# Performance work log

Measured on AMD Instinct MI355X. Metric: run time of the kernel, lower is better.

Reference implementation:

```python
import jax, jax.numpy as jnp
import numpy as np

N_NODES = 100000
N_EDGES = 1600000
D_IN = 128
D_OUT = 128
N_GRAPHS = 256


def setup_inputs() -> dict:
    key = jax.random.key(0)
    k1, k2, k3, k4 = jax.random.split(key, 4)
    H = jax.random.normal(k1, (N_NODES, D_IN), dtype=jnp.float32)
    edge_index = jax.random.randint(k2, (2, N_EDGES), 0, N_NODES, dtype=jnp.int64)
    batch = jnp.sort(jax.random.randint(k3, (N_NODES,), 0, N_GRAPHS, dtype=jnp.int64))
    # Kaiming-normal init: std = sqrt(2 / fan_in)
    W = jax.random.normal(k4, (D_IN, D_OUT), dtype=jnp.float32) * np.float32(np.sqrt(2.0 / D_IN))
    return {"H": H, "edge_index": edge_index, "batch": batch, "W": W}


def reference(H, edge_index, batch, W):
    N = H.shape[0]
    src, dst = edge_index[0], edge_index[1]
    # message passing: gather source features, scatter_add into destinations
    agg = jax.ops.segment_sum(H[src], dst, num_segments=N)  # [N, D]
    out = H + agg
    # virtual node: per-graph mean, broadcast back to nodes
    sums = jax.ops.segment_sum(out, batch, num_segments=N_GRAPHS)            # [G, D]
    counts = jax.ops.segment_sum(jnp.ones((N, 1), out.dtype), batch,
                                 num_segments=N_GRAPHS)                       # [G, 1]
    vmean = sums / jnp.maximum(counts, 1.0)
    out = out + vmean[batch]
    # dense transform + activation
    return jax.nn.relu(out @ W)
```

## Files before the change

### kernel.cpp

```cpp
#include <hip/hip_runtime.h>

#define DIM 128
#define NGRAPH 256

#define CHUNK 512
#define CHB 9
#define MAXNB 256
#define EPB 4096
#define EPT (EPB / 256)
#define FCAP 14336

typedef __attribute__((ext_vector_type(8))) short short8;
typedef __attribute__((ext_vector_type(4))) float f32x4;

__device__ inline unsigned int bpack2(float lo, float hi) {
  unsigned int ul = __float_as_uint(lo);
  unsigned int uh = __float_as_uint(hi);
  ul = (ul + 0x7fffu + ((ul >> 16) & 1u)) >> 16;
  uh = (uh + 0x7fffu + ((uh >> 16) & 1u)) & 0xffff0000u;
  return ul | uh;
}

__global__ __launch_bounds__(256) void k_h2b(const float4* __restrict__ in,
    uint2* __restrict__ ob, int n4) {
  int i = blockIdx.x * 256 + threadIdx.x;
  if (i < n4) {
    float4 a = in[i];
    uint2 r;
    r.x = bpack2(a.x, a.y);
    r.y = bpack2(a.z, a.w);
    ob[i] = r;
  }
}

__global__ __launch_bounds__(256) void k_bhist(const int* __restrict__ dst,
    unsigned short* __restrict__ bh, int E) {
  __shared__ unsigned int hist[MAXNB];
  int blk = blockIdx.x, t = threadIdx.x;
  hist[t] = 0;
  __syncthreads();
  int base = blk * EPB;
#pragma unroll
  for (int i = 0; i < EPT; ++i) {
    int e = base + i * 256 + t;
    if (e < E) atomicAdd(&hist[((unsigned)dst[e]) >> CHB], 1);
  }
  __syncthreads();
  bh[(size_t)blk * MAXNB + t] = (unsigned short)hist[t];
}

__global__ __launch_bounds__(256) void k_bscan(unsigned short* __restrict__ bh,
    unsigned int* __restrict__ btot, int NBLK) {
  __shared__ unsigned int tmp[256];
  int b = blockIdx.x, t = threadIdx.x;
  int i0 = 2 * t, i1 = 2 * t + 1;
  unsigned int a0 = (i0 < NBLK) ? bh[(size_t)i0 * MAXNB + b] : 0u;
  unsigned int a1 = (i1 < NBLK) ? bh[(size_t)i1 * MAXNB + b] : 0u;
  unsigned int ps = a0 + a1;
  tmp[t] = ps;
  __syncthreads();
  for (int off = 1; off < 256; off <<= 1) {
    unsigned int x = (t >= off) ? tmp[t - off] : 0u;
    __syncthreads();
    tmp[t] += x;
    __syncthreads();
  }
  unsigned int ex = tmp[t] - ps;
  if (i0 < NBLK) bh[(size_t)i0 * MAXNB + b] = (unsigned short)ex;
  if (i1 < NBLK) bh[(size_t)i1 * MAXNB + b] = (unsigned short)(ex + a0);
  if (t == 255) btot[b] = tmp[255];
}

__global__ __launch_bounds__(256) void k_bscan2(const unsigned int* __restrict__ btot,
    unsigned int* __restrict__ bbase, int* __restrict__ offs, int N, int E) {
  __shared__ unsigned int s[256];
  int t = threadIdx.x;
  unsigned int v = btot[t];
  s[t] = v;
  __syncthreads();
  for (int off = 1; off < 256; off <<= 1) {
    unsigned int x = (t >= off) ? s[t - off] : 0u;
    __syncthreads();
    s[t] += x;
    __syncthreads();
  }
  bbase[t] = s[t] - v;
  if (t == 255) { bbase[256] = s[255]; offs[N] = E; }
}

__global__ __launch_bounds__(256) void k_part(const int* __restrict__ src,
    const int* __restrict__ dst, const unsigned short* __restrict__ bh,
    const unsigned int* __restrict__ bbase, unsigned int* __restrict__ pack, int E) {
  __shared__ unsigned int hist[MAXNB];
  __shared__ unsigned int sc[MAXNB];
  __shared__ unsigned int gbase[MAXNB];
  __shared__ unsigned int lpack[EPB];
  __shared__ unsigned short lbkt[EPB];
  __shared__ unsigned int totS;
  int blk = blockIdx.x, t = threadIdx.x;
  hist[t] = 0;
  __syncthreads();

  int base = blk * EPB;
  unsigned int pk[EPT];
  int bk[EPT];
  unsigned int rk[EPT];
#pragma unroll
  for (int i = 0; i < EPT; ++i) {
    int e = base + i * 256 + t;
    if (e < E) {
      unsigned int s = (unsigned)src[e], d = (unsigned)dst[e];
      pk[i] = (s << CHB) | (d & (CHUNK - 1));
      int b = (int)(d >> CHB);
      bk[i] = b;
      rk[i] = atomicAdd(&hist[b], 1u);
    } else {
      bk[i] = -1;
    }
  }
  __syncthreads();

  unsigned int c = hist[t];
  sc[t] = c;
  __syncthreads();
  for (int off = 1; off < 256; off <<= 1) {
    unsigned int x = (t >= off) ? sc[t - off] : 0u;
    __syncthreads();
    sc[t] += x;
    __syncthreads();
  }
  if (t == 255) totS = sc[255];
  hist[t] = sc[t] - c;
  gbase[t] = bbase[t] + (unsigned int)bh[(size_t)blk * MAXNB + t];
  __syncthreads();

#pragma unroll
  for (int i = 0; i < EPT; ++i) {
    if (bk[i] >= 0) {
      unsigned int slot = hist[bk[i]] + rk[i];
      lpack[slot] = pk[i];
      lbkt[slot] = (unsigned short)bk[i];
    }
  }
  __syncthreads();

  unsigned int tot = totS;
  for (unsigned int s = t; s < tot; s += 256) {
    int b = lbkt[s];
    unsigned int local = s - hist[b];
    pack[gbase[b] + local] = lpack[s];
  }
}

__global__ __launch_bounds__(256) void k_fine(unsigned int* __restrict__ pack,
    const unsigned int* __restrict__ bbase, int* __restrict__ offs, int N) {
  __shared__ unsigned int lp[FCAP];
  __shared__ unsigned int cnt[CHUNK];
  __shared__ unsigned int cur[CHUNK];
  __shared__ unsigned int tmp[256];
  int b = blockIdx.x, t = threadIdx.x;
  unsigned int lo = bbase[b], hi = bbase[b + 1];
  int n = (int)(hi - lo);
  if (n > FCAP) n = FCAP;
  cnt[2 * t] = 0; cnt[2 * t + 1] = 0;
  __syncthreads();
  for (int i = t; i < n; i += 256) {
    unsigned int p = pack[lo + i];
    lp[i] = p;
    atomicAdd(&cnt[p & (CHUNK - 1)], 1u);
  }
  __syncthreads();
  unsigned int c0 = cnt[2 * t], c1 = cnt[2 * t + 1];
  unsigned int ps = c0 + c1;
  tmp[t] = ps;
  __syncthreads();
  for (int off = 1; off < 256; off <<= 1) {
    unsigned int x = (t >= off) ? tmp[t - off] : 0u;
    __syncthreads();
    tmp[t] += x;
    __syncthreads();
  }
  unsigned int ex = tmp[t] - ps;
  cur[2 * t] = ex;
  cur[2 * t + 1] = ex + c0;
  __syncthreads();
  int nb0 = b * CHUNK;
#pragma unroll
  for (int j = t; j < CHUNK; j += 256) {
    int node = nb0 + j;
    if (node < N) offs[node] = (int)(lo + cur[j]);
  }
  __syncthreads();
  for (int i = t; i < n; i += 256) {
    unsigned int p = lp[i];
    unsigned int r = atomicAdd(&cur[p & (CHUNK - 1)], 1u);
    pack[lo + r] = p;
  }
}

__device__ inline void bacc(uint2 v, float4& a) {
  a.x += __uint_as_float(v.x << 16);
  a.y += __uint_as_float(v.x & 0xffff0000u);
  a.z += __uint_as_float(v.y << 16);
  a.w += __uint_as_float(v.y & 0xffff0000u);
}

__global__ __launch_bounds__(256) void k_gatherb(const float* __restrict__ H,
    const uint2* __restrict__ Hb, const int* __restrict__ offs,
    const unsigned int* __restrict__ pack, float* __restrict__ out, int n) {
  int gid = blockIdx.x * 256 + threadIdx.x;
  int node = gid >> 6;
  if (node >= n) return;
  int lane = threadIdx.x & 63;
  int half = lane >> 5, q = lane & 31;
  float4 A = {0,0,0,0}, B = {0,0,0,0}, C = {0,0,0,0}, D = {0,0,0,0};
  int beg = offs[node], end = offs[node + 1];
  int j = beg + half;
  for (; j + 6 < end; j += 8) {
    uint2 v0 = Hb[(size_t)(pack[j + 0] >> CHB) * 32 + q];
    uint2 v1 = Hb[(size_t)(pack[j + 2] >> CHB) * 32 + q];
    uint2 v2 = Hb[(size_t)(pack[j + 4] >> CHB) * 32 + q];
    uint2 v3 = Hb[(size_t)(pack[j + 6] >> CHB) * 32 + q];
    bacc(v0, A); bacc(v1, B); bacc(v2, C); bacc(v3, D);
  }
  for (; j < end; j += 2) bacc(Hb[(size_t)(pack[j] >> CHB) * 32 + q], A);
  A.x += B.x + (C.x + D.x);
  A.y += B.y + (C.y + D.y);
  A.z += B.z + (C.z + D.z);
  A.w += B.w + (C.w + D.w);
  A.x += __shfl_xor(A.x, 32);
  A.y += __shfl_xor(A.y, 32);
  A.z += __shfl_xor(A.z, 32);
  A.w += __shfl_xor(A.w, 32);
  if (half == 0) {
    float4 b4 = ((const float4*)H)[(size_t)node * 32 + q];
    float4 r;
    r.x = b4.x + A.x; r.y = b4.y + A.y; r.z = b4.z + A.z; r.w = b4.w + A.w;
    ((float4*)out)[(size_t)node * 32 + q] = r;
  }
}

__global__ __launch_bounds__(256) void k_gather(const float* __restrict__ H,
    const int* __restrict__ offs, const unsigned int* __restrict__ pack,
    float* __restrict__ out, int n) {
  int gid = blockIdx.x * 256 + threadIdx.x;
  int node = gid >> 6;
  if (node >= n) return;
  int lane = threadIdx.x & 63;
  const float2* H2 = (const float2*)H;
  float2 base = H2[(size_t)node * 64 + lane];
  float2 s0 = {0.f, 0.f}, s1 = {0.f, 0.f}, s2 = {0.f, 0.f}, s3 = {0.f, 0.f};
  int beg = offs[node], end = offs[node + 1];
  int j = beg;
  for (; j + 4 <= end; j += 4) {
    int n0 = (int)(pack[j + 0] >> CHB);
    int n1 = (int)(pack[j + 1] >> CHB);
    int n2 = (int)(pack[j + 2] >> CHB);
    int n3 = (int)(pack[j + 3] >> CHB);
    float2 v0 = H2[(size_t)n0 * 64 + lane];
    float2 v1 = H2[(size_t)n1 * 64 + lane];
    float2 v2 = H2[(size_t)n2 * 64 + lane];
    float2 v3 = H2[(size_t)n3 * 64 + lane];
    s0.x += v0.x; s0.y += v0.y;
    s1.x += v1.x; s1.y += v1.y;
    s2.x += v2.x; s2.y += v2.y;
    s3.x += v3.x; s3.y += v3.y;
  }
  for (; j < end; ++j) {
    float2 v = H2[(size_t)(pack[j] >> CHB) * 64 + lane];
    s0.x += v.x; s0.y += v.y;
  }
  float2 r;
  r.x = base.x + ((s0.x + s1.x) + (s2.x + s3.x));
  r.y = base.y + ((s0.y + s1.y) + (s2.y + s3.y));
  ((float2*)out)[(size_t)node * 64 + lane] = r;
}

__global__ __launch_bounds__(256) void k_init(const float4* __restrict__ s,
                                              float4* __restrict__ d, int n4) {
  int i = blockIdx.x * 256 + threadIdx.x;
  if (i < n4) d[i] = s[i];
}

__global__ __launch_bounds__(256) void k_scatter(const float* __restrict__ H,
    const int* __restrict__ src, const int* __restrict__ dst,
    float* __restrict__ out, int nE) {
  long long idx = (long long)blockIdx.x * 256 + threadIdx.x;
  int e = (int)(idx >> 5);
  if (e >= nE) return;
  int q = (int)(idx & 31);
  int s = src[e];
  int t = dst[e];
  const float4 h = *(const float4*)(H + (size_t)s * DIM + q * 4);
  float* o = out + (size_t)t * DIM + q * 4;
  unsafeAtomicAdd(o + 0, h.x);
  unsafeAtomicAdd(o + 1, h.y);
  unsafeAtomicAdd(o + 2, h.z);
  unsafeAtomicAdd(o + 3, h.w);
}

__global__ __launch_bounds__(256) void k_vmean4(const float* __restrict__ x,
    const int* __restrict__ batch, float* __restrict__ vmean, int n) {
  int g = blockIdx.x >> 2, c = blockIdx.x & 3;
  int lo = 0, hi = n;
  while (lo < hi) { int m = (lo + hi) >> 1; if (batch[m] < g) lo = m + 1; else hi = m; }
  int start = lo;
  hi = n;
  while (lo < hi) { int m = (lo + hi) >> 1; if (batch[m] < g + 1) lo = m + 1; else hi = m; }
  int end = lo;

  int t = threadIdx.x, rg = t >> 3, s = t & 7;
  int d4 = c * 8 + s;
  const float4* x4 = (const float4*)x;
  float4 acc = {0,0,0,0};
  for (int r = start + rg; r < end; r += 32) {
    float4 v = x4[(size_t)r * 32 + d4];
    acc.x += v.x; acc.y += v.y; acc.z += v.z; acc.w += v.w;
  }
  __shared__ float4 sd[256];
  sd[t] = acc;
  __syncthreads();
  for (int off = 16; off >= 1; off >>= 1) {
    if (rg < off) {
      float4 o = sd[t + off * 8];
      acc.x += o.x; acc.y += o.y; acc.z += o.z; acc.w += o.w;
      sd[t] = acc;
    }
    __syncthreads();
  }
  if (rg == 0) {
    float cnt = fmaxf((float)(end - start), 1.0f);
    float4 r;
    r.x = acc.x / cnt; r.y = acc.y / cnt; r.z = acc.z / cnt; r.w = acc.w / cnt;
    ((float4*)vmean)[g * 32 + d4] = r;
  }
}

__global__ __launch_bounds__(256) void k_wprep(const float* __restrict__ W,
                                               uint4* __restrict__ wt) {
  int gid = blockIdx.x * 256 + threadIdx.x;
  int col = gid >> 4, chunk = gid & 15;
  float f[8];
#pragma unroll
  for (int j = 0; j < 8; ++j) f[j] = W[(chunk * 8 + j) * DIM + col];
  uint4 u;
  u.x = bpack2(f[0], f[1]);
  u.y = bpack2(f[2], f[3]);
  u.z = bpack2(f[4], f[5]);
  u.w = bpack2(f[6], f[7]);
  wt[col * 16 + (chunk ^ (col & 7))] = u;
}

__global__ __launch_bounds__(256) void k_mfma(float* __restrict__ io,
    const int* __restrict__ batch, const float* __restrict__ vmean,
    const uint4* __restrict__ wt, int n) {
  __shared__ uint4 WtL[2048];
  int tid = threadIdx.x;
#pragma unroll
  for (int j = 0; j < 8; ++j) WtL[tid + 256 * j] = wt[tid + 256 * j];
  __syncthreads();

  int wid = tid >> 6;
  int lane = tid & 63;
  int q = lane & 15, hi = lane >> 4;
  int row0 = blockIdx.x * 128 + wid * 32;

  f32x4 acc[2][8];
#pragma unroll
  for (int m = 0; m < 2; ++m)
#pragma unroll
    for (int nn = 0; nn < 8; ++nn) acc[m][nn] = (f32x4){0.f, 0.f, 0.f, 0.f};

  bool okm[2];
  const float4* xrow[2];
  const float4* vrow[2];
#pragma unroll
  for (int m = 0; m < 2; ++m) {
    int row = row0 + m * 16 + q;
    bool ok = row < n;
    okm[m] = ok;
    int g = ok ? batch[row] : 0;
    xrow[m] = (const float4*)io + (size_t)row * 32;
    vrow[m] = (const float4*)vmean + (size_t)g * 32;
  }

  for (int kk = 0; kk < 4; ++kk) {
    short8 Bf[8];
#pragma unroll
    for (int nn = 0; nn < 8; ++nn) {
      int colrow = nn * 16 + q;
      int idx = colrow * 16 + ((kk * 4 + hi) ^ (colrow & 7));
      Bf[nn] = *(short8*)&WtL[idx];
    }
    short8 Af[2];
#pragma unroll
    for (int m = 0; m < 2; ++m) {
      float4 x0 = {0,0,0,0}, x1 = {0,0,0,0};
      if (okm[m]) {
        int c = kk * 8 + hi * 2;
        float4 a0 = xrow[m][c], a1 = xrow[m][c + 1];
        float4 v0 = vrow[m][c], v1 = vrow[m][c + 1];
        x0.x = a0.x + v0.x; x0.y = a0.y + v0.y; x0.z = a0.z + v0.z; x0.w = a0.w + v0.w;
        x1.x = a1.x + v1.x; x1.y = a1.y + v1.y; x1.z = a1.z + v1.z; x1.w = a1.w + v1.w;
      }
      uint4 u;
      u.x = bpack2(x0.x, x0.y);
      u.y = bpack2(x0.z, x0.w);
      u.z = bpack2(x1.x, x1.y);
      u.w = bpack2(x1.z, x1.w);
      Af[m] = *(short8*)&u;
    }
#pragma unroll
    for (int nn = 0; nn < 8; ++nn) {
      acc[0][nn] = __builtin_amdgcn_mfma_f32_16x16x32_bf16(Af[0], Bf[nn], acc[0][nn], 0, 0, 0);
      acc[1][nn] = __builtin_amdgcn_mfma_f32_16x16x32_bf16(Af[1], Bf[nn], acc[1][nn], 0, 0, 0);
    }
  }

#pragma unroll
  for (int m = 0; m < 2; ++m) {
    int grow0 = row0 + m * 16 + hi * 4;
#pragma unroll
    for (int nn = 0; nn < 8; ++nn) {
      int gcol = nn * 16 + q;
      f32x4 c = acc[m][nn];
#pragma unroll
      for (int r = 0; r < 4; ++r) {
        int grow = grow0 + r;
        if (grow < n) io[(size_t)grow * DIM + gcol] = fmaxf(c[r], 0.f);
      }
    }
  }
}

#define TRR 64
__global__ __launch_bounds__(256) void k_gemm(float* __restrict__ io,
    const int* __restrict__ batch, const float* __restrict__ vmean,
    const float* __restrict__ W, int n) {
  __shared__ float xs[TRR][DIM + 1];
  __shared__ float Wl[DIM][64];
  int tid = threadIdx.x;
  int row0 = blockIdx.x * TRR;

  for (int i = tid; i < TRR * 32; i += 256) {
    int r = i >> 5, c4 = i & 31;
    int row = row0 + r;
    float4 a;
    if (row < n) {
      int g = batch[row];
      float4 xv = *((const float4*)(io + (size_t)row * DIM) + c4);
      float4 vv = *((const float4*)(vmean + (size_t)g * DIM) + c4);
      a.x = xv.x + vv.x; a.y = xv.y + vv.y; a.z = xv.z + vv.z; a.w = xv.w + vv.w;
    } else {
      a.x = a.y = a.z = a.w = 0.f;
    }
    xs[r][c4 * 4 + 0] = a.x;
    xs[r][c4 * 4 + 1] = a.y;
    xs[r][c4 * 4 + 2] = a.z;
    xs[r][c4 * 4 + 3] = a.w;
  }

  int cg = tid & 15;
  int rg = tid >> 4;
  float acc[4][4];

  for (int jh = 0; jh < 2; ++jh) {
    __syncthreads();
    for (int i = tid; i < DIM * 16; i += 256) {
      int k = i >> 4, c4 = i & 15;
      *(float4*)&Wl[k][c4 * 4] =
          *(const float4*)(W + (size_t)k * DIM + jh * 64 + c4 * 4);
    }
    __syncthreads();

#pragma unroll
    for (int a = 0; a < 4; ++a)
#pragma unroll
      for (int b = 0; b < 4; ++b) acc[a][b] = 0.f;

    for (int k = 0; k < DIM; ++k) {
      float4 wv = *(const float4*)&Wl[k][cg * 4];
#pragma unroll
      for (int a = 0; a < 4; ++a) {
        float xv = xs[rg * 4 + a][k];
        acc[a][0] += xv * wv.x;
        acc[a][1] += xv * wv.y;
        acc[a][2] += xv * wv.z;
        acc[a][3] += xv * wv.w;
      }
    }

#pragma unroll
    for (int a = 0; a < 4; ++a) {
      int row = row0 + rg * 4 + a;
      if (row < n) {
        float4 o;
        o.x = fmaxf(acc[a][0], 0.f);
        o.y = fmaxf(acc[a][1], 0.f);
        o.z = fmaxf(acc[a][2], 0.f);
        o.w = fmaxf(acc[a][3], 0.f);
        *(float4*)(io + (size_t)row * DIM + jh * 64 + cg * 4) = o;
      }
    }
  }
}

extern "C" void kernel_launch(void* const* d_in, const int* in_sizes, int n_in,
                              void* d_out, int out_size, void* d_ws, size_t ws_size,
                              hipStream_t stream) {
  const float* H     = (const float*)d_in[0];
  const int*   ei    = (const int*)d_in[1];
  const int*   batch = (const int*)d_in[2];
  const float* W     = (const float*)d_in[3];
  float* out = (float*)d_out;

  int N = in_sizes[0] / DIM;
  int E = in_sizes[1] / 2;
  const int* src = ei;
  const int* dst = ei + E;

  int NB   = (N + CHUNK - 1) >> CHB;
  int NBLK = (E + EPB - 1) / EPB;

  size_t o = 0;
  auto carve = [&](size_t bytes) -> void* {
    void* p = (char*)d_ws + o;
    o = (o + bytes + 255) & ~(size_t)255;
    return p;
  };
  unsigned int*   pack  = (unsigned int*)carve((size_t)E * 4);
  int*            offs  = (int*)carve(((size_t)N + 1) * 4);
  unsigned short* bh    = (unsigned short*)carve((size_t)NBLK * MAXNB * 2);
  unsigned int*   btot  = (unsigned int*)carve(MAXNB * 4);
  unsigned int*   bbase = (unsigned int*)carve((MAXNB + 1) * 4);
  size_t o_csr = o;
  uint2*          Hb    = (uint2*)carve((size_t)N * DIM * 2);
  size_t o_bf = o;
  uint4*          wt    = (uint4*)carve((size_t)DIM * DIM * 2);
  size_t o_wt = o;
  float* vmean = (float*)bh;

  bool csr_ok = (o_csr <= ws_size) && (NB >= 1) && (NB <= MAXNB) &&
                (NBLK <= 512) && ((size_t)NBLK * MAXNB * 2 >= (size_t)NGRAPH * DIM * 4) &&
                (E / NB <= 8192);
  bool bf_ok = csr_ok && (o_bf <= ws_size);
  bool wt_ok = bf_ok && (o_wt <= ws_size) && (DIM == 128);

  if (csr_ok) {
    k_bhist<<<NBLK, 256, 0, stream>>>(dst, bh, E);
    k_bscan<<<MAXNB, 256, 0, stream>>>(bh, btot, NBLK);
    k_bscan2<<<1, 256, 0, stream>>>(btot, bbase, offs, N, E);
    k_part<<<NBLK, 256, 0, stream>>>(src, dst, bh, bbase, pack, E);
    k_fine<<<NB, 256, 0, stream>>>(pack, bbase, offs, N);
    long long gthreads = (long long)N * 64;
    if (bf_ok) {
      int n4 = N * DIM / 4;
      k_h2b<<<(n4 + 255) / 256, 256, 0, stream>>>((const float4*)H, Hb, n4);
      k_gatherb<<<(int)((gthreads + 255) / 256), 256, 0, stream>>>(H, Hb, offs, pack, out, N);
    } else {
      k_gather<<<(int)((gthreads + 255) / 256), 256, 0, stream>>>(H, offs, pack, out, N);
    }
  } else {
    vmean = (float*)d_ws;
    int n4 = N * DIM / 4;
    k_init<<<(n4 + 255) / 256, 256, 0, stream>>>((const float4*)H, (float4*)out, n4);
    long long sthreads = (long long)E * 32;
    k_scatter<<<(int)((sthreads + 255) / 256), 256, 0, stream>>>(H, src, dst, out, E);
  }

  k_vmean4<<<NGRAPH * 4, 256, 0, stream>>>(out, batch, vmean, N);

  if (wt_ok) {
    k_wprep<<<8, 256, 0, stream>>>(W, wt);
    k_mfma<<<(N + 127) / 128, 256, 0, stream>>>(out, batch, vmean, wt, N);
  } else {
    k_gemm<<<(N + TRR - 1) / TRR, 256, 0, stream>>>(out, batch, vmean, W, N);
  }
}
```

Baseline: 168.2 us.

## Split bf16 feature gather into two column-half passes and fuse histogram with conversion

Stores the bf16 copy of H as two column halves (64 features each) and runs the neighbour gather twice, once per half, with four edge groups of 16 lanes per node. Each pass touches a 12.8MB table, so the randomly gathered rows are more likely to stay in cache. The bf16 conversion and the destination-bucket histogram now run in one launch instead of two. In exchange, the pack and offs arrays are read twice and there is one more gather launch.

```diff
diff --git a/kernel.cpp b/kernel.cpp
--- a/kernel.cpp
+++ b/kernel.cpp
@@ -21,15 +21,33 @@
   return ul | uh;
 }
 
-__global__ __launch_bounds__(256) void k_h2b(const float4* __restrict__ in,
-    uint2* __restrict__ ob, int n4) {
-  int i = blockIdx.x * 256 + threadIdx.x;
+__global__ __launch_bounds__(256) void k_prep(const float4* __restrict__ H4,
+    uint2* __restrict__ Hb0, uint2* __restrict__ Hb1, int n4,
+    const int* __restrict__ dst, unsigned short* __restrict__ bh, int E,
+    int NBLK) {
+  __shared__ unsigned int hist[MAXNB];
+  int blk = blockIdx.x, t = threadIdx.x;
+  int i = blk * 256 + t;
   if (i < n4) {
-    float4 a = in[i];
+    float4 a = H4[i];
     uint2 r;
     r.x = bpack2(a.x, a.y);
     r.y = bpack2(a.z, a.w);
-    ob[i] = r;
+    int node = i >> 5, c4 = i & 31;
+    uint2* dest = (c4 < 16) ? Hb0 : Hb1;
+    dest[(size_t)node * 16 + (c4 & 15)] = r;
+  }
+  if (blk < NBLK) {
+    hist[t] = 0;
+    __syncthreads();
+    int base = blk * EPB;
+#pragma unroll
+    for (int k = 0; k < EPT; ++k) {
+      int e = base + k * 256 + t;
+      if (e < E) atomicAdd(&hist[((unsigned)dst[e]) >> CHB], 1);
+    }
+    __syncthreads();
+    bh[(size_t)blk * MAXNB + t] = (unsigned short)hist[t];
   }
 }
 
@@ -205,38 +223,43 @@
   a.w += __uint_as_float(v.y & 0xffff0000u);
 }
 
-__global__ __launch_bounds__(256) void k_gatherb(const float* __restrict__ H,
-    const uint2* __restrict__ Hb, const int* __restrict__ offs,
-    const unsigned int* __restrict__ pack, float* __restrict__ out, int n) {
+__global__ __launch_bounds__(256) void k_gather2(const float* __restrict__ H,
+    const uint2* __restrict__ Hbp, const int* __restrict__ offs,
+    const unsigned int* __restrict__ pack, float* __restrict__ out,
+    int n, int half) {
   int gid = blockIdx.x * 256 + threadIdx.x;
   int node = gid >> 6;
   if (node >= n) return;
   int lane = threadIdx.x & 63;
-  int half = lane >> 5, q = lane & 31;
+  int grp = lane >> 4, q = lane & 15;
   float4 A = {0,0,0,0}, B = {0,0,0,0}, C = {0,0,0,0}, D = {0,0,0,0};
   int beg = offs[node], end = offs[node + 1];
-  int j = beg + half;
-  for (; j + 6 < end; j += 8) {
-    uint2 v0 = Hb[(size_t)(pack[j + 0] >> CHB) * 32 + q];
-    uint2 v1 = Hb[(size_t)(pack[j + 2] >> CHB) * 32 + q];
-    uint2 v2 = Hb[(size_t)(pack[j + 4] >> CHB) * 32 + q];
-    uint2 v3 = Hb[(size_t)(pack[j + 6] >> CHB) * 32 + q];
+  int j = beg + grp;
+  for (; j + 12 < end; j += 16) {
+    uint2 v0 = Hbp[(size_t)(pack[j + 0] >> CHB) * 16 + q];
+    uint2 v1 = Hbp[(size_t)(pack[j + 4] >> CHB) * 16 + q];
+    uint2 v2 = Hbp[(size_t)(pack[j + 8] >> CHB) * 16 + q];
+    uint2 v3 = Hbp[(size_t)(pack[j + 12] >> CHB) * 16 + q];
     bacc(v0, A); bacc(v1, B); bacc(v2, C); bacc(v3, D);
   }
-  for (; j < end; j += 2) bacc(Hb[(size_t)(pack[j] >> CHB) * 32 + q], A);
+  for (; j < end; j += 4) bacc(Hbp[(size_t)(pack[j] >> CHB) * 16 + q], A);
   A.x += B.x + (C.x + D.x);
   A.y += B.y + (C.y + D.y);
   A.z += B.z + (C.z + D.z);
   A.w += B.w + (C.w + D.w);
+  A.x += __shfl_xor(A.x, 16);
+  A.y += __shfl_xor(A.y, 16);
+  A.z += __shfl_xor(A.z, 16);
+  A.w += __shfl_xor(A.w, 16);
   A.x += __shfl_xor(A.x, 32);
   A.y += __shfl_xor(A.y, 32);
   A.z += __shfl_xor(A.z, 32);
   A.w += __shfl_xor(A.w, 32);
-  if (half == 0) {
-    float4 b4 = ((const float4*)H)[(size_t)node * 32 + q];
+  if (grp == 0) {
+    float4 b4 = ((const float4*)H)[(size_t)node * 32 + half * 16 + q];
     float4 r;
     r.x = b4.x + A.x; r.y = b4.y + A.y; r.z = b4.z + A.z; r.w = b4.w + A.w;
-    ((float4*)out)[(size_t)node * 32 + q] = r;
+    ((float4*)out)[(size_t)node * 32 + half * 16 + q] = r;
   }
 }
 
@@ -534,7 +557,8 @@
   unsigned int*   btot  = (unsigned int*)carve(MAXNB * 4);
   unsigned int*   bbase = (unsigned int*)carve((MAXNB + 1) * 4);
   size_t o_csr = o;
-  uint2*          Hb    = (uint2*)carve((size_t)N * DIM * 2);
+  uint2*          Hb0   = (uint2*)carve((size_t)N * DIM);
+  uint2*          Hb1   = (uint2*)carve((size_t)N * DIM);
   size_t o_bf = o;
   uint4*          wt    = (uint4*)carve((size_t)DIM * DIM * 2);
   size_t o_wt = o;
@@ -547,18 +571,25 @@
   bool wt_ok = bf_ok && (o_wt <= ws_size) && (DIM == 128);
 
   if (csr_ok) {
-    k_bhist<<<NBLK, 256, 0, stream>>>(dst, bh, E);
+    if (bf_ok) {
+      int n4 = N * DIM / 4;
+      int gprep = (n4 + 255) / 256;
+      if (gprep < NBLK) gprep = NBLK;
+      k_prep<<<gprep, 256, 0, stream>>>((const float4*)H, Hb0, Hb1, n4, dst, bh, E, NBLK);
+    } else {
+      k_bhist<<<NBLK, 256, 0, stream>>>(dst, bh, E);
+    }
     k_bscan<<<MAXNB, 256, 0, stream>>>(bh, btot, NBLK);
     k_bscan2<<<1, 256, 0, stream>>>(btot, bbase, offs, N, E);
     k_part<<<NBLK, 256, 0, stream>>>(src, dst, bh, bbase, pack, E);
     k_fine<<<NB, 256, 0, stream>>>(pack, bbase, offs, N);
     long long gthreads = (long long)N * 64;
+    int gblocks = (int)((gthreads + 255) / 256);
     if (bf_ok) {
-      int n4 = N * DIM / 4;
-      k_h2b<<<(n4 + 255) / 256, 256, 0, stream>>>((const float4*)H, Hb, n4);
-      k_gatherb<<<(int)((gthreads + 255) / 256), 256, 0, stream>>>(H, Hb, offs, pack, out, N);
+      k_gather2<<<gblocks, 256, 0, stream>>>(H, Hb0, offs, pack, out, N, 0);
+      k_gather2<<<gblocks, 256, 0, stream>>>(H, Hb1, offs, pack, out, N, 1);
     } else {
-      k_gather<<<(int)((gthreads + 255) / 256), 256, 0, stream>>>(H, offs, pack, out, N);
+      k_gather<<<gblocks, 256, 0, stream>>>(H, offs, pack, out, N);
     }
   } else {
     vmean = (float*)d_ws;
```

Result: slower. 191.9 us (+14.1%).

## Store aggregated node features as bf16 and fuse bf16 conversion into histogram kernel

Applied to the files above, without the earlier changes.

Fuses the H-to-bf16 conversion with the destination-bucket histogram into one kernel launch. The gather now writes H+agg as bf16 into a new workspace buffer instead of fp32. The per-graph mean and the MFMA GEMM read that bf16 buffer, which roughly halves the intermediate traffic between those three stages. The cost is extra rounding: the self term and the aggregated sum are both rounded to bf16 before the mean is computed. The fp32 fallback gather loop is also trimmed from 4 to 2 accumulators.

```diff
diff --git a/kernel.cpp b/kernel.cpp
--- a/kernel.cpp
+++ b/kernel.cpp
@@ -21,15 +21,40 @@
   return ul | uh;
 }
 
-__global__ __launch_bounds__(256) void k_h2b(const float4* __restrict__ in,
-    uint2* __restrict__ ob, int n4) {
-  int i = blockIdx.x * 256 + threadIdx.x;
+__device__ inline float4 bunpack4(uint2 v) {
+  float4 r;
+  r.x = __uint_as_float(v.x << 16);
+  r.y = __uint_as_float(v.x & 0xffff0000u);
+  r.z = __uint_as_float(v.y << 16);
+  r.w = __uint_as_float(v.y & 0xffff0000u);
+  return r;
+}
+
+__global__ __launch_bounds__(256) void k_prep(const float4* __restrict__ H4,
+    uint2* __restrict__ Hb, int n4,
+    const int* __restrict__ dst, unsigned short* __restrict__ bh, int E,
+    int NBLK) {
+  __shared__ unsigned int hist[MAXNB];
+  int blk = blockIdx.x, t = threadIdx.x;
+  int i = blk * 256 + t;
   if (i < n4) {
-    float4 a = in[i];
+    float4 a = H4[i];
     uint2 r;
     r.x = bpack2(a.x, a.y);
     r.y = bpack2(a.z, a.w);
-    ob[i] = r;
+    Hb[i] = r;
+  }
+  if (blk < NBLK) {
+    hist[t] = 0;
+    __syncthreads();
+    int base = blk * EPB;
+#pragma unroll
+    for (int k = 0; k < EPT; ++k) {
+      int e = base + k * 256 + t;
+      if (e < E) atomicAdd(&hist[((unsigned)dst[e]) >> CHB], 1);
+    }
+    __syncthreads();
+    bh[(size_t)blk * MAXNB + t] = (unsigned short)hist[t];
   }
 }
 
@@ -203,6 +228,42 @@
   a.y += __uint_as_float(v.x & 0xffff0000u);
   a.z += __uint_as_float(v.y << 16);
   a.w += __uint_as_float(v.y & 0xffff0000u);
+}
+
+__global__ __launch_bounds__(256) void k_gatherbx(const uint2* __restrict__ Hb,
+    const int* __restrict__ offs, const unsigned int* __restrict__ pack,
+    uint2* __restrict__ Hx, int n) {
+  int gid = blockIdx.x * 256 + threadIdx.x;
+  int node = gid >> 6;
+  if (node >= n) return;
+  int lane = threadIdx.x & 63;
+  int half = lane >> 5, q = lane & 31;
+  float4 A = {0,0,0,0}, B = {0,0,0,0}, C = {0,0,0,0}, D = {0,0,0,0};
+  int beg = offs[node], end = offs[node + 1];
+  int j = beg + half;
+  for (; j + 6 < end; j += 8) {
+    uint2 v0 = Hb[(size_t)(pack[j + 0] >> CHB) * 32 + q];
+    uint2 v1 = Hb[(size_t)(pack[j + 2] >> CHB) * 32 + q];
+    uint2 v2 = Hb[(size_t)(pack[j + 4] >> CHB) * 32 + q];
+    uint2 v3 = Hb[(size_t)(pack[j + 6] >> CHB) * 32 + q];
+    bacc(v0, A); bacc(v1, B); bacc(v2, C); bacc(v3, D);
+  }
+  for (; j < end; j += 2) bacc(Hb[(size_t)(pack[j] >> CHB) * 32 + q], A);
+  A.x += B.x + (C.x + D.x);
+  A.y += B.y + (C.y + D.y);
+  A.z += B.z + (C.z + D.z);
+  A.w += B.w + (C.w + D.w);
+  A.x += __shfl_xor(A.x, 32);
+  A.y += __shfl_xor(A.y, 32);
+  A.z += __shfl_xor(A.z, 32);
+  A.w += __shfl_xor(A.w, 32);
+  if (half == 0) {
+    float4 b4 = bunpack4(Hb[(size_t)node * 32 + q]);
+    uint2 o;
+    o.x = bpack2(b4.x + A.x, b4.y + A.y);
+    o.y = bpack2(b4.z + A.z, b4.w + A.w);
+    Hx[(size_t)node * 32 + q] = o;
+  }
 }
 
 __global__ __launch_bounds__(256) void k_gatherb(const float* __restrict__ H,
@@ -249,30 +310,22 @@
   int lane = threadIdx.x & 63;
   const float2* H2 = (const float2*)H;
   float2 base = H2[(size_t)node * 64 + lane];
-  float2 s0 = {0.f, 0.f}, s1 = {0.f, 0.f}, s2 = {0.f, 0.f}, s3 = {0.f, 0.f};
+  float2 s0 = {0.f, 0.f}, s1 = {0.f, 0.f};
   int beg = offs[node], end = offs[node + 1];
   int j = beg;
-  for (; j + 4 <= end; j += 4) {
-    int n0 = (int)(pack[j + 0] >> CHB);
-    int n1 = (int)(pack[j + 1] >> CHB);
-    int n2 = (int)(pack[j + 2] >> CHB);
-    int n3 = (int)(pack[j + 3] >> CHB);
-    float2 v0 = H2[(size_t)n0 * 64 + lane];
-    float2 v1 = H2[(size_t)n1 * 64 + lane];
-    float2 v2 = H2[(size_t)n2 * 64 + lane];
-    float2 v3 = H2[(size_t)n3 * 64 + lane];
+  for (; j + 2 <= end; j += 2) {
+    float2 v0 = H2[(size_t)(pack[j + 0] >> CHB) * 64 + lane];
+    float2 v1 = H2[(size_t)(pack[j + 1] >> CHB) * 64 + lane];
     s0.x += v0.x; s0.y += v0.y;
     s1.x += v1.x; s1.y += v1.y;
-    s2.x += v2.x; s2.y += v2.y;
-    s3.x += v3.x; s3.y += v3.y;
   }
   for (; j < end; ++j) {
     float2 v = H2[(size_t)(pack[j] >> CHB) * 64 + lane];
     s0.x += v.x; s0.y += v.y;
   }
   float2 r;
-  r.x = base.x + ((s0.x + s1.x) + (s2.x + s3.x));
-  r.y = base.y + ((s0.y + s1.y) + (s2.y + s3.y));
+  r.x = base.x + s0.x + s1.x;
+  r.y = base.y + s0.y + s1.y;
   ((float2*)out)[(size_t)node * 64 + lane] = r;
 }
 
@@ -299,6 +352,42 @@
   unsafeAtomicAdd(o + 3, h.w);
 }
 
+__global__ __launch_bounds__(256) void k_vmean4x(const uint2* __restrict__ hx,
+    const int* __restrict__ batch, float* __restrict__ vmean, int n) {
+  int g = blockIdx.x >> 2, c = blockIdx.x & 3;
+  int lo = 0, hi = n;
+  while (lo < hi) { int m = (lo + hi) >> 1; if (batch[m] < g) lo = m + 1; else hi = m; }
+  int start = lo;
+  hi = n;
+  while (lo < hi) { int m = (lo + hi) >> 1; if (batch[m] < g + 1) lo = m + 1; else hi = m; }
+  int end = lo;
+
+  int t = threadIdx.x, rg = t >> 3, s = t & 7;
+  int d4 = c * 8 + s;
+  float4 acc = {0,0,0,0};
+  for (int r = start + rg; r < end; r += 32) {
+    float4 v = bunpack4(hx[(size_t)r * 32 + d4]);
+    acc.x += v.x; acc.y += v.y; acc.z += v.z; acc.w += v.w;
+  }
+  __shared__ float4 sd[256];
+  sd[t] = acc;
+  __syncthreads();
+  for (int off = 16; off >= 1; off >>= 1) {
+    if (rg < off) {
+      float4 o = sd[t + off * 8];
+      acc.x += o.x; acc.y += o.y; acc.z += o.z; acc.w += o.w;
+      sd[t] = acc;
+    }
+    __syncthreads();
+  }
+  if (rg == 0) {
+    float cnt = fmaxf((float)(end - start), 1.0f);
+    float4 r;
+    r.x = acc.x / cnt; r.y = acc.y / cnt; r.z = acc.z / cnt; r.w = acc.w / cnt;
+    ((float4*)vmean)[g * 32 + d4] = r;
+  }
+}
+
 __global__ __launch_bounds__(256) void k_vmean4(const float* __restrict__ x,
     const int* __restrict__ batch, float* __restrict__ vmean, int n) {
   int g = blockIdx.x >> 2, c = blockIdx.x & 3;
@@ -349,6 +438,87 @@
   u.z = bpack2(f[4], f[5]);
   u.w = bpack2(f[6], f[7]);
   wt[col * 16 + (chunk ^ (col & 7))] = u;
+}
+
+__global__ __launch_bounds__(256) void k_mfmax(const uint4* __restrict__ Hx,
+    float* __restrict__ io, const int* __restrict__ batch,
+    const float* __restrict__ vmean, const uint4* __restrict__ wt, int n) {
+  __shared__ uint4 WtL[2048];
+  int tid = threadIdx.x;
+#pragma unroll
+  for (int j = 0; j < 8; ++j) WtL[tid + 256 * j] = wt[tid + 256 * j];
+  __syncthreads();
+
+  int wid = tid >> 6;
+  int lane = tid & 63;
+  int q = lane & 15, hi = lane >> 4;
+  int row0 = blockIdx.x * 128 + wid * 32;
+
+  f32x4 acc[2][8];
+#pragma unroll
+  for (int m = 0; m < 2; ++m)
+#pragma unroll
+    for (int nn = 0; nn < 8; ++nn) acc[m][nn] = (f32x4){0.f, 0.f, 0.f, 0.f};
+
+  bool okm[2];
+  const uint4* xrow[2];
+  const float4* vrow[2];
+#pragma unroll
+  for (int m = 0; m < 2; ++m) {
+    int row = row0 + m * 16 + q;
+    bool ok = row < n;
+    okm[m] = ok;
+    int g = ok ? batch[row] : 0;
+    xrow[m] = Hx + (size_t)row * 16;
+    vrow[m] = (const float4*)vmean + (size_t)g * 32;
+  }
+
+  for (int kk = 0; kk < 4; ++kk) {
+    short8 Bf[8];
+#pragma unroll
+    for (int nn = 0; nn < 8; ++nn) {
+      int colrow = nn * 16 + q;
+      int idx = colrow * 16 + ((kk * 4 + hi) ^ (colrow & 7));
+      Bf[nn] = *(short8*)&WtL[idx];
+    }
+    short8 Af[2];
+#pragma unroll
+    for (int m = 0; m < 2; ++m) {
+      uint4 u = {0, 0, 0, 0};
+      if (okm[m]) {
+        uint4 xv = xrow[m][kk * 4 + hi];
+        float4 x0 = bunpack4(*(uint2*)&xv.x);
+        float4 x1 = bunpack4(*(uint2*)&xv.z);
+        int c = kk * 8 + hi * 2;
+        float4 v0 = vrow[m][c], v1 = vrow[m][c + 1];
+        u.x = bpack2(x0.x + v0.x, x0.y + v0.y);
+        u.y = bpack2(x0.z + v0.z, x0.w + v0.w);
+        u.z = bpack2(x1.x + v1.x, x1.y + v1.y);
+        u.w = bpack2(x1.z + v1.z, x1.w + v1.w);
+      }
+      Af[m] = *(short8*)&u;
+    }
+#pragma unroll
+    for (int nn = 0; nn < 8; ++nn) {
+      acc[0][nn] = __builtin_amdgcn_mfma_f32_16x16x32_bf16(Af[0], Bf[nn], acc[0][nn], 0, 0, 0);
+      acc[1][nn] = __builtin_amdgcn_mfma_f32_16x16x32_bf16(Af[1], Bf[nn], acc[1][nn], 0, 0, 0);
+    }
+  }
+
+#pragma unroll
+  for (int m = 0; m < 2; ++m) {
+    int grow0 = row0 + m * 16 + hi * 4;
+#pragma unroll
+    for (int nn = 0; nn < 8; ++nn) {
+      int gcol = nn * 16 + q;
+      f32x4 c = acc[m][nn];
+#pragma unroll
+      for (int r = 0; r < 4; ++r) {
+        int grow = grow0 + r;
+        if (grow < n) io[(size_t)grow * DIM + gcol] = fmaxf(c[r], 0.f);
+      }
+    }
+  }
 }
 
 __global__ __launch_bounds__(256) void k_mfma(float* __restrict__ io,
@@ -538,6 +708,8 @@
   size_t o_bf = o;
   uint4*          wt    = (uint4*)carve((size_t)DIM * DIM * 2);
   size_t o_wt = o;
+  uint2*          Hx    = (uint2*)carve((size_t)N * DIM * 2);
+  size_t o_hx = o;
   float* vmean = (float*)bh;
 
   bool csr_ok = (o_csr <= ws_size) && (NB >= 1) && (NB <= MAXNB) &&
@@ -545,20 +717,34 @@
                 (E / NB <= 8192);
   bool bf_ok = csr_ok && (o_bf <= ws_size);
   bool wt_ok = bf_ok && (o_wt <= ws_size) && (DIM == 128);
+  bool hx_ok = wt_ok && (o_hx <= ws_size);
 
   if (csr_ok) {
-    k_bhist<<<NBLK, 256, 0, stream>>>(dst, bh, E);
+    if (bf_ok) {
+      int n4 = N * DIM / 4;
+      int gprep = (n4 + 255) / 256;
+      if (gprep < NBLK) gprep = NBLK;
+      k_prep<<<gprep, 256, 0, stream>>>((const float4*)H, Hb, n4, dst, bh, E, NBLK);
+    } else {
+      k_bhist<<<NBLK, 256, 0, stream>>>(dst, bh, E);
+    }
     k_bscan<<<MAXNB, 256, 0, stream>>>(bh, btot, NBLK);
     k_bscan2<<<1, 256, 0, stream>>>(btot, bbase, offs, N, E);
     k_part<<<NBLK, 256, 0, stream>>>(src, dst, bh, bbase, pack, E);
     k_fine<<<NB, 256, 0, stream>>>(pack, bbase, offs, N);
     long long gthreads = (long long)N * 64;
+    int gblocks = (int)((gthreads + 255) / 256);
+    if (hx_ok) {
+      k_gatherbx<<<gblocks, 256, 0, stream>>>(Hb, offs, pack, Hx, N);
+      k_vmean4x<<<NGRAPH * 4, 256, 0, stream>>>(Hx, batch, vmean, N);
+      k_wprep<<<8, 256, 0, stream>>>(W, wt);
+      k_mfmax<<<(N + 127) / 128, 256, 0, stream>>>((const uint4*)Hx, out, batch, vmean, wt, N);
+      return;
+    }
     if (bf_ok) {
-      int n4 = N * DIM / 4;
-      k_h2b<<<(n4 + 255) / 256, 256, 0, stream>>>((const float4*)H, Hb, n4);
-      k_gatherb<<<(int)((gthreads + 255) / 256), 256, 0, stream>>>(H, Hb, offs, pack, out, N);
+      k_gatherb<<<gblocks, 256, 0, stream>>>(H, Hb, offs, pack, out, N);
     } else {
-      k_gather<<<(int)((gthreads + 255) / 256), 256, 0, stream>>>(H, offs, pack, out, N);
+      k_gather<<<gblocks, 256, 0, stream>>>(H, offs, pack, out, N);
     }
   } else {
     vmean = (float*)d_ws;
```

After: 159.2 us (median of 2 runs). 1.06x faster.
